# Performance work log

Hardware: AMD Instinct MI355X
Metric: run time of the kernel (lower is better)

## Reference

```python
import jax, jax.numpy as jnp
import numpy as np
from jax import lax

B = 65536

def _conv3(x, w, b):
    # x: [B,Cin,H,W], w: [Cout,Cin,3,3] (OIHW), SAME padding, stride 1
    y = lax.conv_general_dilated(x, w, (1, 1), 'SAME',
                                 dimension_numbers=('NCHW', 'OIHW', 'NCHW'))
    return y + b[None, :, None, None]

def _gru_cell(x, h, wu, bu, wr, br, wo, bo):
    s = jnp.concatenate([x, h], axis=1)
    update = jax.nn.sigmoid(_conv3(s, wu, bu))
    reset = jax.nn.sigmoid(_conv3(s, wr, br))
    out = jnp.tanh(_conv3(jnp.concatenate([x, h * reset], axis=1), wo, bo))
    return h * (1.0 - update) + out * update

def _mk_cell_params(key, cin, ch):
    ks = jax.random.split(key, 6)
    fan = (cin + ch) * 9
    sc = 1.0 / np.sqrt(fan)
    p = {}
    for i, g in enumerate(['u', 'r', 'o']):
        p['w' + g] = jax.random.normal(ks[2 * i], (ch, cin + ch, 3, 3), jnp.float32) * sc
        p['b' + g] = jax.random.normal(ks[2 * i + 1], (ch,), jnp.float32) * sc
    return p

def setup_inputs() -> dict:
    key = jax.random.key(0)
    k_in, k1, k2, k3, kd1, kd2 = jax.random.split(key, 6)
    inputs = jax.random.normal(k_in, (B, 1, 3, 3), jnp.float32)
    p1 = _mk_cell_params(k1, 1, 32)
    p2 = _mk_cell_params(k2, 32, 64)
    p3 = _mk_cell_params(k3, 64, 16)
    wd = jax.random.normal(kd1, (9, 16 * 3 * 3), jnp.float32) * (1.0 / 12.0)
    bd = jax.random.normal(kd2, (9,), jnp.float32) * (1.0 / 12.0)
    out = {'inputs': inputs, 'wd': wd, 'bd': bd}
    for i, p in enumerate([p1, p2, p3], start=1):
        for k, v in p.items():
            out[f'{k[0]}{i}{k[1]}'] = v  # e.g. w1u, b1u
    return out

def reference(inputs, wd, bd,
              w1u, b1u, w1r, b1r, w1o, b1o,
              w2u, b2u, w2r, b2r, w2o, b2o,
              w3u, b3u, w3r, b3r, w3o, b3o):
    b = inputs.shape[0]
    h1 = jnp.zeros((b, 32, 3, 3), inputs.dtype)
    h2 = jnp.zeros((b, 64, 3, 3), inputs.dtype)
    h3 = jnp.zeros((b, 16, 3, 3), inputs.dtype)
    x1 = _gru_cell(inputs, h1, w1u, b1u, w1r, b1r, w1o, b1o)
    x2 = _gru_cell(x1, h2, w2u, b2u, w2r, b2r, w2o, b2o)
    x3 = _gru_cell(x2, h3, w3u, b3u, w3r, b3r, w3o, b3o)
    out = x3.reshape(b, -1) @ wd.T + bd
    return (out, x1, x2, x3)
```

## Files before the change

kernel.cpp:

```cpp
#include <hip/hip_runtime.h>

#define BATCH 65536

typedef __attribute__((ext_vector_type(8))) short bf16x8;
typedef __attribute__((ext_vector_type(4))) float f32x4;

__device__ __forceinline__ unsigned short f2bf(float f) {
  unsigned int u = __float_as_uint(f);
  u += 0x7fffu + ((u >> 16) & 1u);
  return (unsigned short)(u >> 16);
}
__device__ __forceinline__ unsigned pack_trunc(float lo, float hi) {
  return __builtin_amdgcn_perm(__float_as_uint(hi), __float_as_uint(lo), 0x07060302u);
}

__device__ __forceinline__ float gru_act(float u, float o) {
  u = fmaxf(u, -60.0f);
  o = fmaxf(o, -30.0f);
  float a  = __expf(-u);
  float a2 = __expf(-2.0f * o);
  return (1.0f - a2) * __builtin_amdgcn_rcpf((1.0f + a) * (1.0f + a2));
}

__device__ __forceinline__ float conv_tap(const float* __restrict__ w, int co, int ci,
                                          int p, int q, int CINTOT) {
  int pi = p / 3, pj = p % 3, qi = q / 3, qj = q % 3;
  int di = qi - pi + 1, dj = qj - pj + 1;
  if ((unsigned)di < 3u && (unsigned)dj < 3u)
    return w[((co * CINTOT + ci) * 3 + di) * 3 + dj];
  return 0.0f;
}

__global__ void build_bt(const float* __restrict__ wu, const float* __restrict__ wo,
                         unsigned short* __restrict__ BT, int COUT, int CINX, int CINTOT) {
  int NG = COUT * 9, K = CINX * 9;
  int total = 2 * NG * K;
  int e = blockIdx.x * 256 + threadIdx.x;
  if (e >= total) return;
  int g = e / (NG * K);
  int rem = e - g * (NG * K);
  int n = rem / K, k = rem - n * K;
  BT[e] = f2bf(conv_tap(g ? wo : wu, n / 9, k / 9, n % 9, k % 9, CINTOT));
}

__global__ void build_a1(const float* __restrict__ wu, const float* __restrict__ wo,
                         float* __restrict__ A1) {
  int e = blockIdx.x * 256 + threadIdx.x;
  if (e >= 5184) return;
  int g = e / 2592;
  int rem = e - g * 2592;
  int q = rem / 288, c = rem - q * 288;
  A1[e] = conv_tap(g ? wo : wu, c / 9, 0, c % 9, q, 33);
}

#define OFF_X1L 0
#define OFF_X3L 0
#define OFF_WL 20480
#define OFF_BLB 25664
#define OFF_BL 40960
#define OFF_XL 65536
#define OFF_AL 65536
#define SMEM_BYTES 69632

__global__ __launch_bounds__(256, 2) void megafused(
    const float* __restrict__ xin, const float* __restrict__ A1,
    const float* __restrict__ b1u, const float* __restrict__ b1o,
    const unsigned short* __restrict__ BT2,
    const float* __restrict__ b2u, const float* __restrict__ b2o,
    const unsigned short* __restrict__ BT3,
    const float* __restrict__ b3u, const float* __restrict__ b3o,
    const float* __restrict__ wd, const float* __restrict__ bd,
    float* __restrict__ x1, float* __restrict__ x2,
    float* __restrict__ x3, float* __restrict__ out) {
  __shared__ __align__(16) char smem[SMEM_BYTES];
  char* x1l = smem + OFF_X1L;
  char* Bl = smem + OFF_BL;
  char* Al = smem + OFF_AL;
  unsigned short* x3l = (unsigned short*)(smem + OFF_X3L);
  float* xl = (float*)(smem + OFF_XL);
  float* wl = (float*)(smem + OFF_WL);
  float* blb = (float*)(smem + OFF_BLB);

  const int tid = threadIdx.x;
  const int lane = tid & 63;
  const int wid = tid >> 6;
  const int lrow = lane & 15;
  const int jc = lane >> 4;
  const int r0 = blockIdx.x * 64;
  const int srow = tid >> 2, spart = tid & 3;

  unsigned toffB2[6];
  char* wB2[6];
#pragma unroll
  for (int ci = 0; ci < 6; ++ci) {
    int row = ci * 64 + srow;
    int bg = (row < 192) ? row : (384 + row);
    toffB2[ci] = (unsigned)bg * 288u + spart * 8;
    wB2[ci] = Bl + row * 64 + ((spart ^ ((row >> 1) & 3)) << 4);
  }

  for (int c = tid; c < 576; c += 256) xl[(c / 9) * 12 + (c % 9)] = xin[(size_t)r0 * 9 + c];
  __syncthreads();

  bf16x8 pf[6];
#pragma unroll
  for (int ci = 0; ci < 6; ++ci) pf[ci] = *(const bf16x8*)(BT2 + toffB2[ci]);

  {
    float au0[9], ao0[9], au1[9], ao1[9];
    const int c1 = tid, c2 = tid + 256;
    const bool has2 = (c2 < 288);
#pragma unroll
    for (int q = 0; q < 9; ++q) {
      au0[q] = A1[q * 288 + c1];
      ao0[q] = A1[2592 + q * 288 + c1];
      au1[q] = has2 ? A1[q * 288 + c2] : 0.0f;
      ao1[q] = has2 ? A1[2592 + q * 288 + c2] : 0.0f;
    }
    float bu0 = b1u[c1 / 9], bo0 = b1o[c1 / 9];
    float bu1 = has2 ? b1u[c2 / 9] : 0.0f;
    float bo1 = has2 ? b1o[c2 / 9] : 0.0f;
    for (int r = 0; r < 64; ++r) {
      const float4 xv0 = *(const float4*)&xl[r * 12];
      const float4 xv1 = *(const float4*)&xl[r * 12 + 4];
      const float x8 = xl[r * 12 + 8];
      float u0 = bu0, o0 = bo0, u1 = bu1, o1 = bo1;
      u0 = fmaf(au0[0], xv0.x, u0); o0 = fmaf(ao0[0], xv0.x, o0);
      u0 = fmaf(au0[1], xv0.y, u0); o0 = fmaf(ao0[1], xv0.y, o0);
      u0 = fmaf(au0[2], xv0.z, u0); o0 = fmaf(ao0[2], xv0.z, o0);
      u0 = fmaf(au0[3], xv0.w, u0); o0 = fmaf(ao0[3], xv0.w, o0);
      u0 = fmaf(au0[4], xv1.x, u0); o0 = fmaf(ao0[4], xv1.x, o0);
      u0 = fmaf(au0[5], xv1.y, u0); o0 = fmaf(ao0[5], xv1.y, o0);
      u0 = fmaf(au0[6], xv1.z, u0); o0 = fmaf(ao0[6], xv1.z, o0);
      u0 = fmaf(au0[7], xv1.w, u0); o0 = fmaf(ao0[7], xv1.w, o0);
      u0 = fmaf(au0[8], x8, u0);    o0 = fmaf(ao0[8], x8, o0);
      float v0 = gru_act(u0, o0);
      x1[(size_t)(r0 + r) * 288 + c1] = v0;
      *(unsigned short*)(x1l + r * 640 + (((c1 >> 3) ^ (r & 7)) << 4) + (c1 & 7) * 2) =
          (unsigned short)(__float_as_uint(v0) >> 16);
      if (has2) {
        u1 = fmaf(au1[0], xv0.x, u1); o1 = fmaf(ao1[0], xv0.x, o1);
        u1 = fmaf(au1[1], xv0.y, u1); o1 = fmaf(ao1[1], xv0.y, o1);
        u1 = fmaf(au1[2], xv0.z, u1); o1 = fmaf(ao1[2], xv0.z, o1);
        u1 = fmaf(au1[3], xv0.w, u1); o1 = fmaf(ao1[3], xv0.w, o1);
        u1 = fmaf(au1[4], xv1.x, u1); o1 = fmaf(ao1[4], xv1.x, o1);
        u1 = fmaf(au1[5], xv1.y, u1); o1 = fmaf(ao1[5], xv1.y, o1);
        u1 = fmaf(au1[6], xv1.z, u1); o1 = fmaf(ao1[6], xv1.z, o1);
        u1 = fmaf(au1[7], xv1.w, u1); o1 = fmaf(ao1[7], xv1.w, o1);
        u1 = fmaf(au1[8], x8, u1);    o1 = fmaf(ao1[8], x8, o1);
        float v1 = gru_act(u1, o1);
        x1[(size_t)(r0 + r) * 288 + c2] = v1;
        *(unsigned short*)(x1l + r * 640 + (((c2 >> 3) ^ (r & 7)) << 4) + (c2 & 7) * 2) =
            (unsigned short)(__float_as_uint(v1) >> 16);
      }
    }
  }

  {
    const char* rB[2][3];
#pragma unroll
    for (int g = 0; g < 2; ++g)
#pragma unroll
      for (int f = 0; f < 3; ++f) {
        int rb = g * 192 + (wid * 3 + f) * 16 + lrow;
        rB[g][f] = Bl + rb * 64 + ((jc ^ ((rb >> 1) & 3)) << 4);
      }
    const char* aBase[4];
    int aXor[4];
#pragma unroll
    for (int m = 0; m < 4; ++m) {
      int row = m * 16 + lrow;
      aBase[m] = x1l + row * 640;
      aXor[m] = row & 7;
    }

    f32x4 acc[4][2][3] = {};
    for (int s = 0; s < 27; ++s) {
      const int kt = s - (s / 9) * 9;
#pragma unroll
      for (int ci = 0; ci < 6; ++ci) *(bf16x8*)wB2[ci] = pf[ci];
      __syncthreads();
      if (s < 26) {
        int ns = s + 1;
        unsigned uoff = (unsigned)(ns / 9) * 55296u + (unsigned)(ns % 9) * 32u;
#pragma unroll
        for (int ci = 0; ci < 6; ++ci)
          pf[ci] = *(const bf16x8*)(BT2 + uoff + toffB2[ci]);
      }
      bf16x8 af[4];
      const int c8 = kt * 4 + jc;
#pragma unroll
      for (int m = 0; m < 4; ++m)
        af[m] = *(const bf16x8*)(aBase[m] + ((c8 ^ aXor[m]) << 4));
      bf16x8 bfr[2][3];
#pragma unroll
      for (int g = 0; g < 2; ++g)
#pragma unroll
        for (int f = 0; f < 3; ++f) bfr[g][f] = *(const bf16x8*)rB[g][f];
#pragma unroll
      for (int m = 0; m < 4; ++m)
#pragma unroll
        for (int g = 0; g < 2; ++g)
#pragma unroll
          for (int f = 0; f < 3; ++f)
            acc[m][g][f] = __builtin_amdgcn_mfma_f32_16x16x32_bf16(
                af[m], bfr[g][f], acc[m][g][f], 0, 0, 0);
      if (kt == 8) {
        const int n0 = (s / 9) * 192;
#pragma unroll
        for (int m = 0; m < 4; ++m)
#pragma unroll
          for (int f = 0; f < 3; ++f) {
            int n = n0 + (wid * 3 + f) * 16 + lrow;
            float bU = b2u[n / 9], bO = b2o[n / 9];
            f32x4 u = acc[m][0][f], o = acc[m][1][f];
#pragma unroll
            for (int t = 0; t < 4; ++t) {
              int r = r0 + m * 16 + jc * 4 + t;
              x2[(size_t)r * 576 + n] = gru_act(u[t] + bU, o[t] + bO);
            }
            acc[m][0][f] = (f32x4){0.f, 0.f, 0.f, 0.f};
            acc[m][1][f] = (f32x4){0.f, 0.f, 0.f, 0.f};
          }
      }
      __syncthreads();
    }
  }

  {
    unsigned toffB3[5];
    char* wB3[5];
#pragma unroll
    for (int j = 0; j < 5; ++j) {
      int c = j * 256 + tid;
      if (c < 1152) {
        int row = c >> 2, part = c & 3;
        toffB3[j] = (unsigned)row * 576u + part * 8;
        wB3[j] = Bl + row * 64 + ((part ^ ((row >> 1) & 3)) << 4);
      } else {
        toffB3[j] = 0; wB3[j] = Bl;
      }
    }
    const float* pA = x2 + (size_t)(r0 + srow) * 576 + spart * 8;
    char* wAl = Al + srow * 64 + ((spart ^ ((srow >> 1) & 3)) << 4);

    float4 pa0 = *(const float4*)pA;
    float4 pa1 = *(const float4*)(pA + 4);
    bf16x8 pb[5];
#pragma unroll
    for (int j = 0; j < 5; ++j)
      if (j * 256 + tid < 1152) pb[j] = *(const bf16x8*)(BT3 + toffB3[j]);

    for (int c = tid; c < 1296; c += 256) wl[c] = wd[c];
    if (tid < 9) blb[tid] = bd[tid];

    const char* rB3[2][3];
#pragma unroll
    for (int g = 0; g < 2; ++g)
#pragma unroll
      for (int f = 0; f < 3; ++f) {
        int rb = g * 144 + (wid * 3 + f) * 16 + lrow;
        rB3[g][f] = Bl + rb * 64 + ((jc ^ ((rb >> 1) & 3)) << 4);
      }
    const char* rA3[4];
#pragma unroll
    for (int m = 0; m < 4; ++m) {
      int row = m * 16 + lrow;
      rA3[m] = Al + row * 64 + ((jc ^ ((row >> 1) & 3)) << 4);
    }

    f32x4 acc[4][2][3] = {};
    for (int kt = 0; kt < 18; ++kt) {
      uint4 h;
      h.x = pack_trunc(pa0.x, pa0.y);
      h.y = pack_trunc(pa0.z, pa0.w);
      h.z = pack_trunc(pa1.x, pa1.y);
      h.w = pack_trunc(pa1.z, pa1.w);
      *(uint4*)wAl = h;
#pragma unroll
      for (int j = 0; j < 5; ++j)
        if (j * 256 + tid < 1152) *(bf16x8*)wB3[j] = pb[j];
      __syncthreads();
      if (kt < 17) {
        const float* gp = pA + (kt + 1) * 32;
        pa0 = *(const float4*)gp;
        pa1 = *(const float4*)(gp + 4);
        unsigned uoff = (unsigned)(kt + 1) * 32u;
#pragma unroll
        for (int j = 0; j < 5; ++j)
          if (j * 256 + tid < 1152) pb[j] = *(const bf16x8*)(BT3 + uoff + toffB3[j]);
      }
      if (wid < 3) {
        bf16x8 af[4];
#pragma unroll
        for (int m = 0; m < 4; ++m) af[m] = *(const bf16x8*)rA3[m];
        bf16x8 bfr[2][3];
#pragma unroll
        for (int g = 0; g < 2; ++g)
#pragma unroll
          for (int f = 0; f < 3; ++f) bfr[g][f] = *(const bf16x8*)rB3[g][f];
#pragma unroll
        for (int m = 0; m < 4; ++m)
#pragma unroll
          for (int g = 0; g < 2; ++g)
#pragma unroll
            for (int f = 0; f < 3; ++f)
              acc[m][g][f] = __builtin_amdgcn_mfma_f32_16x16x32_bf16(
                  af[m], bfr[g][f], acc[m][g][f], 0, 0, 0);
      }
      __syncthreads();
    }
    if (wid < 3) {
#pragma unroll
      for (int m = 0; m < 4; ++m)
#pragma unroll
        for (int f = 0; f < 3; ++f) {
          int n = (wid * 3 + f) * 16 + lrow;
          float bU = b3u[n / 9], bO = b3o[n / 9];
          f32x4 u = acc[m][0][f], o = acc[m][1][f];
#pragma unroll
          for (int t = 0; t < 4; ++t) {
            int r = m * 16 + jc * 4 + t;
            float v = gru_act(u[t] + bU, o[t] + bO);
            x3[(size_t)(r0 + r) * 144 + n] = v;
            x3l[r * 146 + n] = (unsigned short)(__float_as_uint(v) >> 16);
          }
        }
    }
  }
  __syncthreads();

  if (wid < 3) {
    int drow = lane;
    int jb = wid * 3;
    float s0 = blb[jb], s1 = blb[jb + 1], s2 = blb[jb + 2];
    for (int k = 0; k < 144; k += 2) {
      unsigned pr = *(const unsigned*)&x3l[drow * 146 + k];
      float v0 = __uint_as_float(pr << 16);
      float v1 = __uint_as_float(pr & 0xffff0000u);
      const float2 w0 = *(const float2*)&wl[jb * 144 + k];
      const float2 w1 = *(const float2*)&wl[(jb + 1) * 144 + k];
      const float2 w2 = *(const float2*)&wl[(jb + 2) * 144 + k];
      s0 = fmaf(v0, w0.x, s0); s0 = fmaf(v1, w0.y, s0);
      s1 = fmaf(v0, w1.x, s1); s1 = fmaf(v1, w1.y, s1);
      s2 = fmaf(v0, w2.x, s2); s2 = fmaf(v1, w2.y, s2);
    }
    size_t ob = (size_t)(r0 + drow) * 9 + jb;
    out[ob] = s0; out[ob + 1] = s1; out[ob + 2] = s2;
  }
}

extern "C" void kernel_launch(void* const* d_in, const int* in_sizes, int n_in,
                              void* d_out, int out_size, void* d_ws, size_t ws_size,
                              hipStream_t stream) {
  const float* inputs = (const float*)d_in[0];
  const float* wd  = (const float*)d_in[1];
  const float* bd  = (const float*)d_in[2];
  const float* w1u = (const float*)d_in[3];
  const float* b1u = (const float*)d_in[4];
  const float* w1o = (const float*)d_in[7];
  const float* b1o = (const float*)d_in[8];
  const float* w2u = (const float*)d_in[9];
  const float* b2u = (const float*)d_in[10];
  const float* w2o = (const float*)d_in[13];
  const float* b2o = (const float*)d_in[14];
  const float* w3u = (const float*)d_in[15];
  const float* b3u = (const float*)d_in[16];
  const float* w3o = (const float*)d_in[19];
  const float* b3o = (const float*)d_in[20];

  float* out = (float*)d_out;
  float* x1 = out + (size_t)BATCH * 9;
  float* x2 = x1 + (size_t)BATCH * 288;
  float* x3 = x2 + (size_t)BATCH * 576;

  unsigned short* BT2 = (unsigned short*)d_ws;
  unsigned short* BT3 = BT2 + 331776;
  float* A1 = (float*)((char*)d_ws + 995328);

  build_bt<<<1296, 256, 0, stream>>>(w2u, w2o, BT2, 64, 32, 96);
  build_bt<<<648, 256, 0, stream>>>(w3u, w3o, BT3, 16, 64, 80);
  build_a1<<<21, 256, 0, stream>>>(w1u, w1o, A1);

  megafused<<<BATCH / 64, 256, 0, stream>>>(inputs, A1, b1u, b1o, BT2, b2u, b2o,
                                            BT3, b3u, b3o, wd, bd, x1, x2, x3, out);
}
```

Before: 163.7 us.

## Double block to 512 threads and split MFMA row tiles across wave pairs

Launches the fused GRU kernel with 512 threads per block and splits each block's 64 rows into two 32-row halves across wave groups. Each wave now holds half the MFMA accumulators in layers 2 and 3. The layer-1 scalar conv and the final dense layer are also redistributed so all 8 waves share the work. The goal is more waves in flight to hide latency and fewer registers per wave, at the cost of more threads contending on each block barrier and a launch bound that may force register spills.

```diff
diff --git a/kernel.cpp b/kernel.cpp
--- a/kernel.cpp
+++ b/kernel.cpp
@@ -62,7 +62,7 @@
 #define OFF_AL 65536
 #define SMEM_BYTES 69632
 
-__global__ __launch_bounds__(256, 2) void megafused(
+__global__ __launch_bounds__(512, 4) void megafused(
     const float* __restrict__ xin, const float* __restrict__ A1,
     const float* __restrict__ b1u, const float* __restrict__ b1o,
     const unsigned short* __restrict__ BT2,
@@ -85,73 +85,61 @@
   const int lane = tid & 63;
   const int wid = tid >> 6;
   const int lrow = lane & 15;
-  const int jc = lane >> 4;
+  const int jc = (lane >> 4) & 3;
+  const int mh = wid >> 2;
+  const int cg = wid & 3;
   const int r0 = blockIdx.x * 64;
   const int srow = tid >> 2, spart = tid & 3;
 
-  unsigned toffB2[6];
-  char* wB2[6];
-#pragma unroll
-  for (int ci = 0; ci < 6; ++ci) {
-    int row = ci * 64 + srow;
+  unsigned toffB2[3];
+  char* wB2[3];
+#pragma unroll
+  for (int ci = 0; ci < 3; ++ci) {
+    int row = ci * 128 + srow;
     int bg = (row < 192) ? row : (384 + row);
     toffB2[ci] = (unsigned)bg * 288u + spart * 8;
     wB2[ci] = Bl + row * 64 + ((spart ^ ((row >> 1) & 3)) << 4);
   }
 
-  for (int c = tid; c < 576; c += 256) xl[(c / 9) * 12 + (c % 9)] = xin[(size_t)r0 * 9 + c];
+  for (int c = tid; c < 576; c += 512) xl[(c / 9) * 12 + (c % 9)] = xin[(size_t)r0 * 9 + c];
   __syncthreads();
 
-  bf16x8 pf[6];
-#pragma unroll
-  for (int ci = 0; ci < 6; ++ci) pf[ci] = *(const bf16x8*)(BT2 + toffB2[ci]);
-
-  {
-    float au0[9], ao0[9], au1[9], ao1[9];
-    const int c1 = tid, c2 = tid + 256;
-    const bool has2 = (c2 < 288);
-#pragma unroll
-    for (int q = 0; q < 9; ++q) {
-      au0[q] = A1[q * 288 + c1];
-      ao0[q] = A1[2592 + q * 288 + c1];
-      au1[q] = has2 ? A1[q * 288 + c2] : 0.0f;
-      ao1[q] = has2 ? A1[2592 + q * 288 + c2] : 0.0f;
-    }
-    float bu0 = b1u[c1 / 9], bo0 = b1o[c1 / 9];
-    float bu1 = has2 ? b1u[c2 / 9] : 0.0f;
-    float bo1 = has2 ? b1o[c2 / 9] : 0.0f;
-    for (int r = 0; r < 64; ++r) {
-      const float4 xv0 = *(const float4*)&xl[r * 12];
-      const float4 xv1 = *(const float4*)&xl[r * 12 + 4];
-      const float x8 = xl[r * 12 + 8];
-      float u0 = bu0, o0 = bo0, u1 = bu1, o1 = bo1;
-      u0 = fmaf(au0[0], xv0.x, u0); o0 = fmaf(ao0[0], xv0.x, o0);
-      u0 = fmaf(au0[1], xv0.y, u0); o0 = fmaf(ao0[1], xv0.y, o0);
-      u0 = fmaf(au0[2], xv0.z, u0); o0 = fmaf(ao0[2], xv0.z, o0);
-      u0 = fmaf(au0[3], xv0.w, u0); o0 = fmaf(ao0[3], xv0.w, o0);
-      u0 = fmaf(au0[4], xv1.x, u0); o0 = fmaf(ao0[4], xv1.x, o0);
-      u0 = fmaf(au0[5], xv1.y, u0); o0 = fmaf(ao0[5], xv1.y, o0);
-      u0 = fmaf(au0[6], xv1.z, u0); o0 = fmaf(ao0[6], xv1.z, o0);
-      u0 = fmaf(au0[7], xv1.w, u0); o0 = fmaf(ao0[7], xv1.w, o0);
-      u0 = fmaf(au0[8], x8, u0);    o0 = fmaf(ao0[8], x8, o0);
-      float v0 = gru_act(u0, o0);
-      x1[(size_t)(r0 + r) * 288 + c1] = v0;
-      *(unsigned short*)(x1l + r * 640 + (((c1 >> 3) ^ (r & 7)) << 4) + (c1 & 7) * 2) =
-          (unsigned short)(__float_as_uint(v0) >> 16);
-      if (has2) {
-        u1 = fmaf(au1[0], xv0.x, u1); o1 = fmaf(ao1[0], xv0.x, o1);
-        u1 = fmaf(au1[1], xv0.y, u1); o1 = fmaf(ao1[1], xv0.y, o1);
-        u1 = fmaf(au1[2], xv0.z, u1); o1 = fmaf(ao1[2], xv0.z, o1);
-        u1 = fmaf(au1[3], xv0.w, u1); o1 = fmaf(ao1[3], xv0.w, o1);
-        u1 = fmaf(au1[4], xv1.x, u1); o1 = fmaf(ao1[4], xv1.x, o1);
-        u1 = fmaf(au1[5], xv1.y, u1); o1 = fmaf(ao1[5], xv1.y, o1);
-        u1 = fmaf(au1[6], xv1.z, u1); o1 = fmaf(ao1[6], xv1.z, o1);
-        u1 = fmaf(au1[7], xv1.w, u1); o1 = fmaf(ao1[7], xv1.w, o1);
-        u1 = fmaf(au1[8], x8, u1);    o1 = fmaf(ao1[8], x8, o1);
-        float v1 = gru_act(u1, o1);
-        x1[(size_t)(r0 + r) * 288 + c2] = v1;
-        *(unsigned short*)(x1l + r * 640 + (((c2 >> 3) ^ (r & 7)) << 4) + (c2 & 7) * 2) =
-            (unsigned short)(__float_as_uint(v1) >> 16);
+  bf16x8 pf[3];
+#pragma unroll
+  for (int ci = 0; ci < 3; ++ci) pf[ci] = *(const bf16x8*)(BT2 + toffB2[ci]);
+
+  for (int uu = 0; uu < 3; ++uu) {
+    int u = tid + (uu << 9);
+    if (u < 1152) {
+      int c = u >> 2, rq = u & 3;
+      float au[9], ao[9];
+#pragma unroll
+      for (int q = 0; q < 9; ++q) {
+        au[q] = A1[q * 288 + c];
+        ao[q] = A1[2592 + q * 288 + c];
+      }
+      float bU = b1u[c / 9], bO = b1o[c / 9];
+      const int cbase = c >> 3, cb = (c & 7) * 2;
+#pragma unroll 4
+      for (int i = 0; i < 16; ++i) {
+        int r = (rq << 4) + i;
+        const float4 xv0 = *(const float4*)&xl[r * 12];
+        const float4 xv1 = *(const float4*)&xl[r * 12 + 4];
+        const float x8 = xl[r * 12 + 8];
+        float uacc = bU, oacc = bO;
+        uacc = fmaf(au[0], xv0.x, uacc); oacc = fmaf(ao[0], xv0.x, oacc);
+        uacc = fmaf(au[1], xv0.y, uacc); oacc = fmaf(ao[1], xv0.y, oacc);
+        uacc = fmaf(au[2], xv0.z, uacc); oacc = fmaf(ao[2], xv0.z, oacc);
+        uacc = fmaf(au[3], xv0.w, uacc); oacc = fmaf(ao[3], xv0.w, oacc);
+        uacc = fmaf(au[4], xv1.x, uacc); oacc = fmaf(ao[4], xv1.x, oacc);
+        uacc = fmaf(au[5], xv1.y, uacc); oacc = fmaf(ao[5], xv1.y, oacc);
+        uacc = fmaf(au[6], xv1.z, uacc); oacc = fmaf(ao[6], xv1.z, oacc);
+        uacc = fmaf(au[7], xv1.w, uacc); oacc = fmaf(ao[7], xv1.w, oacc);
+        uacc = fmaf(au[8], x8, uacc);    oacc = fmaf(ao[8], x8, oacc);
+        float v = gru_act(uacc, oacc);
+        x1[(size_t)(r0 + r) * 288 + c] = v;
+        *(unsigned short*)(x1l + r * 640 + ((cbase ^ (r & 7)) << 4) + cb) =
+            (unsigned short)(__float_as_uint(v) >> 16);
       }
     }
   }
@@ -162,35 +150,35 @@
     for (int g = 0; g < 2; ++g)
 #pragma unroll
       for (int f = 0; f < 3; ++f) {
-        int rb = g * 192 + (wid * 3 + f) * 16 + lrow;
+        int rb = g * 192 + (cg * 3 + f) * 16 + lrow;
         rB[g][f] = Bl + rb * 64 + ((jc ^ ((rb >> 1) & 3)) << 4);
       }
-    const char* aBase[4];
-    int aXor[4];
-#pragma unroll
-    for (int m = 0; m < 4; ++m) {
-      int row = m * 16 + lrow;
+    const char* aBase[2];
+    int aXor[2];
+#pragma unroll
+    for (int m = 0; m < 2; ++m) {
+      int row = mh * 32 + m * 16 + lrow;
       aBase[m] = x1l + row * 640;
       aXor[m] = row & 7;
     }
 
-    f32x4 acc[4][2][3] = {};
+    f32x4 acc[2][2][3] = {};
     for (int s = 0; s < 27; ++s) {
       const int kt = s - (s / 9) * 9;
 #pragma unroll
-      for (int ci = 0; ci < 6; ++ci) *(bf16x8*)wB2[ci] = pf[ci];
+      for (int ci = 0; ci < 3; ++ci) *(bf16x8*)wB2[ci] = pf[ci];
       __syncthreads();
       if (s < 26) {
         int ns = s + 1;
         unsigned uoff = (unsigned)(ns / 9) * 55296u + (unsigned)(ns % 9) * 32u;
 #pragma unroll
-        for (int ci = 0; ci < 6; ++ci)
+        for (int ci = 0; ci < 3; ++ci)
           pf[ci] = *(const bf16x8*)(BT2 + uoff + toffB2[ci]);
       }
-      bf16x8 af[4];
+      bf16x8 af[2];
       const int c8 = kt * 4 + jc;
 #pragma unroll
-      for (int m = 0; m < 4; ++m)
+      for (int m = 0; m < 2; ++m)
         af[m] = *(const bf16x8*)(aBase[m] + ((c8 ^ aXor[m]) << 4));
       bf16x8 bfr[2][3];
 #pragma unroll
@@ -198,7 +186,7 @@
 #pragma unroll
         for (int f = 0; f < 3; ++f) bfr[g][f] = *(const bf16x8*)rB[g][f];
 #pragma unroll
-      for (int m = 0; m < 4; ++m)
+      for (int m = 0; m < 2; ++m)
 #pragma unroll
         for (int g = 0; g < 2; ++g)
 #pragma unroll
@@ -208,15 +196,15 @@
       if (kt == 8) {
         const int n0 = (s / 9) * 192;
 #pragma unroll
-        for (int m = 0; m < 4; ++m)
+        for (int m = 0; m < 2; ++m)
 #pragma unroll
           for (int f = 0; f < 3; ++f) {
-            int n = n0 + (wid * 3 + f) * 16 + lrow;
+            int n = n0 + (cg * 3 + f) * 16 + lrow;
             float bU = b2u[n / 9], bO = b2o[n / 9];
             f32x4 u = acc[m][0][f], o = acc[m][1][f];
 #pragma unroll
             for (int t = 0; t < 4; ++t) {
-              int r = r0 + m * 16 + jc * 4 + t;
+              int r = r0 + mh * 32 + m * 16 + jc * 4 + t;
               x2[(size_t)r * 576 + n] = gru_act(u[t] + bU, o[t] + bO);
             }
             acc[m][0][f] = (f32x4){0.f, 0.f, 0.f, 0.f};
@@ -228,30 +216,33 @@
   }
 
   {
-    unsigned toffB3[5];
-    char* wB3[5];
-#pragma unroll
-    for (int j = 0; j < 5; ++j) {
-      int c = j * 256 + tid;
-      if (c < 1152) {
-        int row = c >> 2, part = c & 3;
-        toffB3[j] = (unsigned)row * 576u + part * 8;
-        wB3[j] = Bl + row * 64 + ((part ^ ((row >> 1) & 3)) << 4);
-      } else {
-        toffB3[j] = 0; wB3[j] = Bl;
-      }
-    }
-    const float* pA = x2 + (size_t)(r0 + srow) * 576 + spart * 8;
-    char* wAl = Al + srow * 64 + ((spart ^ ((srow >> 1) & 3)) << 4);
-
-    float4 pa0 = *(const float4*)pA;
-    float4 pa1 = *(const float4*)(pA + 4);
-    bf16x8 pb[5];
-#pragma unroll
-    for (int j = 0; j < 5; ++j)
-      if (j * 256 + tid < 1152) pb[j] = *(const bf16x8*)(BT3 + toffB3[j]);
-
-    for (int c = tid; c < 1296; c += 256) wl[c] = wd[c];
+    unsigned toffB3[3];
+    char* wB3[3];
+    bool vB3[3];
+#pragma unroll
+    for (int ci = 0; ci < 3; ++ci) {
+      int row = ci * 128 + srow;
+      int g = row >= 192;
+      int nloc = row - (g ? 192 : 0);
+      vB3[ci] = (nloc < 144);
+      toffB3[ci] = (unsigned)((g ? 144 : 0) + nloc) * 576u + spart * 8;
+      wB3[ci] = Bl + row * 64 + ((spart ^ ((row >> 1) & 3)) << 4);
+    }
+    const float* pA = x2 + (size_t)(r0 + (tid >> 2)) * 576 + spart * 8;
+    char* wAl = Al + (tid >> 2) * 64 + ((spart ^ (((tid >> 2) >> 1) & 3)) << 4);
+
+    float4 pa0 = {}, pa1 = {};
+    if (tid < 256) {
+      pa0 = *(const float4*)pA;
+      pa1 = *(const float4*)(pA + 4);
+    }
+    bf16x8 pb[3];
+#pragma unroll
+    for (int ci = 0; ci < 3; ++ci)
+      pb[ci] = vB3[ci] ? *(const bf16x8*)(BT3 + toffB3[ci])
+                       : (bf16x8){0, 0, 0, 0, 0, 0, 0, 0};
+
+    for (int c = tid; c < 1296; c += 512) wl[c] = wd[c];
     if (tid < 9) blb[tid] = bd[tid];
 
     const char* rB3[2][3];
@@ -259,68 +250,69 @@
     for (int g = 0; g < 2; ++g)
 #pragma unroll
       for (int f = 0; f < 3; ++f) {
-        int rb = g * 144 + (wid * 3 + f) * 16 + lrow;
+        int rb = g * 192 + (cg * 3 + f) * 16 + lrow;
         rB3[g][f] = Bl + rb * 64 + ((jc ^ ((rb >> 1) & 3)) << 4);
       }
-    const char* rA3[4];
-#pragma unroll
-    for (int m = 0; m < 4; ++m) {
-      int row = m * 16 + lrow;
+    const char* rA3[2];
+#pragma unroll
+    for (int m = 0; m < 2; ++m) {
+      int row = mh * 32 + m * 16 + lrow;
       rA3[m] = Al + row * 64 + ((jc ^ ((row >> 1) & 3)) << 4);
     }
 
-    f32x4 acc[4][2][3] = {};
+    f32x4 acc[2][2][3] = {};
     for (int kt = 0; kt < 18; ++kt) {
-      uint4 h;
-      h.x = pack_trunc(pa0.x, pa0.y);
-      h.y = pack_trunc(pa0.z, pa0.w);
-      h.z = pack_trunc(pa1.x, pa1.y);
-      h.w = pack_trunc(pa1.z, pa1.w);
-      *(uint4*)wAl = h;
-#pragma unroll
-      for (int j = 0; j < 5; ++j)
-        if (j * 256 + tid < 1152) *(bf16x8*)wB3[j] = pb[j];
+      if (tid < 256) {
+        uint4 h;
+        h.x = pack_trunc(pa0.x, pa0.y);
+        h.y = pack_trunc(pa0.z, pa0.w);
+        h.z = pack_trunc(pa1.x, pa1.y);
+        h.w = pack_trunc(pa1.z, pa1.w);
+        *(uint4*)wAl = h;
+      }
+#pragma unroll
+      for (int ci = 0; ci < 3; ++ci) *(bf16x8*)wB3[ci] = pb[ci];
       __syncthreads();
       if (kt < 17) {
-        const float* gp = pA + (kt + 1) * 32;
-        pa0 = *(const float4*)gp;
-        pa1 = *(const float4*)(gp + 4);
+        if (tid < 256) {
+          const float* gp = pA + (kt + 1) * 32;
+          pa0 = *(const float4*)gp;
+          pa1 = *(const float4*)(gp + 4);
+        }
         unsigned uoff = (unsigned)(kt + 1) * 32u;
 #pragma unroll
-        for (int j = 0; j < 5; ++j)
-          if (j * 256 + tid < 1152) pb[j] = *(const bf16x8*)(BT3 + uoff + toffB3[j]);
-      }
-      if (wid < 3) {
-        bf16x8 af[4];
-#pragma unroll
-        for (int m = 0; m < 4; ++m) af[m] = *(const bf16x8*)rA3[m];
-        bf16x8 bfr[2][3];
+        for (int ci = 0; ci < 3; ++ci)
+          if (vB3[ci]) pb[ci] = *(const bf16x8*)(BT3 + uoff + toffB3[ci]);
+      }
+      bf16x8 af[2];
+#pragma unroll
+      for (int m = 0; m < 2; ++m) af[m] = *(const bf16x8*)rA3[m];
+      bf16x8 bfr[2][3];
+#pragma unroll
+      for (int g = 0; g < 2; ++g)
+#pragma unroll
+        for (int f = 0; f < 3; ++f) bfr[g][f] = *(const bf16x8*)rB3[g][f];
+#pragma unroll
+      for (int m = 0; m < 2; ++m)
 #pragma unroll
         for (int g = 0; g < 2; ++g)
 #pragma unroll
-          for (int f = 0; f < 3; ++f) bfr[g][f] = *(const bf16x8*)rB3[g][f];
-#pragma unroll
-        for (int m = 0; m < 4; ++m)
-#pragma unroll
-          for (int g = 0; g < 2; ++g)
-#pragma unroll
-            for (int f = 0; f < 3; ++f)
-              acc[m][g][f] = __builtin_amdgcn_mfma_f32_16x16x32_bf16(
-                  af[m], bfr[g][f], acc[m][g][f], 0, 0, 0);
-      }
+          for (int f = 0; f < 3; ++f)
+            acc[m][g][f] = __builtin_amdgcn_mfma_f32_16x16x32_bf16(
+                af[m], bfr[g][f], acc[m][g][f], 0, 0, 0);
       __syncthreads();
     }
-    if (wid < 3) {
-#pragma unroll
-      for (int m = 0; m < 4; ++m)
+    if (cg < 3) {
+#pragma unroll
+      for (int m = 0; m < 2; ++m)
 #pragma unroll
         for (int f = 0; f < 3; ++f) {
-          int n = (wid * 3 + f) * 16 + lrow;
+          int n = (cg * 3 + f) * 16 + lrow;
           float bU = b3u[n / 9], bO = b3o[n / 9];
           f32x4 u = acc[m][0][f], o = acc[m][1][f];
 #pragma unroll
           for (int t = 0; t < 4; ++t) {
-            int r = m * 16 + jc * 4 + t;
+            int r = mh * 32 + m * 16 + jc * 4 + t;
             float v = gru_act(u[t] + bU, o[t] + bO);
             x3[(size_t)(r0 + r) * 144 + n] = v;
             x3l[r * 146 + n] = (unsigned short)(__float_as_uint(v) >> 16);
@@ -330,23 +322,31 @@
   }
   __syncthreads();
 
-  if (wid < 3) {
-    int drow = lane;
-    int jb = wid * 3;
-    float s0 = blb[jb], s1 = blb[jb + 1], s2 = blb[jb + 2];
+  {
+    int row = lane;
+    int j = wid;
+    float s = blb[j];
     for (int k = 0; k < 144; k += 2) {
-      unsigned pr = *(const unsigned*)&x3l[drow * 146 + k];
+      unsigned pr = *(const unsigned*)&x3l[row * 146 + k];
       float v0 = __uint_as_float(pr << 16);
       float v1 = __uint_as_float(pr & 0xffff0000u);
-      const float2 w0 = *(const float2*)&wl[jb * 144 + k];
-      const float2 w1 = *(const float2*)&wl[(jb + 1) * 144 + k];
-      const float2 w2 = *(const float2*)&wl[(jb + 2) * 144 + k];
-      s0 = fmaf(v0, w0.x, s0); s0 = fmaf(v1, w0.y, s0);
-      s1 = fmaf(v0, w1.x, s1); s1 = fmaf(v1, w1.y, s1);
-      s2 = fmaf(v0, w2.x, s2); s2 = fmaf(v1, w2.y, s2);
-    }
-    size_t ob = (size_t)(r0 + drow) * 9 + jb;
-    out[ob] = s0; out[ob + 1] = s1; out[ob + 2] = s2;
+      const float2 w0 = *(const float2*)&wl[j * 144 + k];
+      s = fmaf(v0, w0.x, s);
+      s = fmaf(v1, w0.y, s);
+    }
+    out[(size_t)(r0 + row) * 9 + j] = s;
+    if (tid < 64) {
+      float s8 = blb[8];
+      for (int k = 0; k < 144; k += 2) {
+        unsigned pr = *(const unsigned*)&x3l[row * 146 + k];
+        float v0 = __uint_as_float(pr << 16);
+        float v1 = __uint_as_float(pr & 0xffff0000u);
+        const float2 w0 = *(const float2*)&wl[8 * 144 + k];
+        s8 = fmaf(v0, w0.x, s8);
+        s8 = fmaf(v1, w0.y, s8);
+      }
+      out[(size_t)(r0 + row) * 9 + 8] = s8;
+    }
   }
 }
 
@@ -382,6 +382,6 @@
   build_bt<<<648, 256, 0, stream>>>(w3u, w3o, BT3, 16, 64, 80);
   build_a1<<<21, 256, 0, stream>>>(w1u, w1o, A1);
 
-  megafused<<<BATCH / 64, 256, 0, stream>>>(inputs, A1, b1u, b1o, BT2, b2u, b2o,
+  megafused<<<BATCH / 64, 512, 0, stream>>>(inputs, A1, b1u, b1o, BT2, b2u, b2o,
                                             BT3, b3u, b3o, wd, bd, x1, x2, x3, out);
 }
```

Result: no change. 163.5 us (-0.1%).

## Compute first GRU layer with bf16 MFMA instead of scalar FMA loops

Applied to the files above, without the earlier changes.

Replaces the first-cell scalar FP32 FMA loop (9 taps per output, 64 rows per thread) with a bf16 MFMA GEMM. The input is padded to K=32 and the cell-1 weights are packed into a bf16 transposed matrix by a new build kernel, then processed in two 144-column chunks. The layer-3 B-tile offsets and the decoder weight staging are reused or moved earlier. This trades some FP32 accuracy in layer 1 for bf16 inputs and raises shared memory use, which could affect occupancy at two blocks per CU.

```diff
diff --git a/kernel.cpp b/kernel.cpp
--- a/kernel.cpp
+++ b/kernel.cpp
@@ -43,14 +43,15 @@
   BT[e] = f2bf(conv_tap(g ? wo : wu, n / 9, k / 9, n % 9, k % 9, CINTOT));
 }
 
-__global__ void build_a1(const float* __restrict__ wu, const float* __restrict__ wo,
-                         float* __restrict__ A1) {
+__global__ void build_bt1(const float* __restrict__ wu, const float* __restrict__ wo,
+                          unsigned short* __restrict__ BT1) {
   int e = blockIdx.x * 256 + threadIdx.x;
-  if (e >= 5184) return;
-  int g = e / 2592;
-  int rem = e - g * 2592;
-  int q = rem / 288, c = rem - q * 288;
-  A1[e] = conv_tap(g ? wo : wu, c / 9, 0, c % 9, q, 33);
+  if (e >= 18432) return;
+  int g = e / 9216;
+  int rem = e - g * 9216;
+  int n = rem / 32, k = rem - n * 32;
+  float v = (k < 9) ? conv_tap(g ? wo : wu, n / 9, 0, n % 9, k, 33) : 0.0f;
+  BT1[e] = f2bf(v);
 }
 
 #define OFF_X1L 0
@@ -58,12 +59,12 @@
 #define OFF_WL 20480
 #define OFF_BLB 25664
 #define OFF_BL 40960
-#define OFF_XL 65536
+#define OFF_XL2 65536
 #define OFF_AL 65536
-#define SMEM_BYTES 69632
+#define SMEM_BYTES 74752
 
 __global__ __launch_bounds__(256, 2) void megafused(
-    const float* __restrict__ xin, const float* __restrict__ A1,
+    const float* __restrict__ xin, const unsigned short* __restrict__ BT1,
     const float* __restrict__ b1u, const float* __restrict__ b1o,
     const unsigned short* __restrict__ BT2,
     const float* __restrict__ b2u, const float* __restrict__ b2o,
@@ -77,7 +78,7 @@
   char* Bl = smem + OFF_BL;
   char* Al = smem + OFF_AL;
   unsigned short* x3l = (unsigned short*)(smem + OFF_X3L);
-  float* xl = (float*)(smem + OFF_XL);
+  float* xl2 = (float*)(smem + OFF_XL2);
   float* wl = (float*)(smem + OFF_WL);
   float* blb = (float*)(smem + OFF_BLB);
 
@@ -90,80 +91,119 @@
   const int srow = tid >> 2, spart = tid & 3;
 
   unsigned toffB2[6];
-  char* wB2[6];
+  int wOffB2[6];
 #pragma unroll
   for (int ci = 0; ci < 6; ++ci) {
     int row = ci * 64 + srow;
     int bg = (row < 192) ? row : (384 + row);
     toffB2[ci] = (unsigned)bg * 288u + spart * 8;
-    wB2[ci] = Bl + row * 64 + ((spart ^ ((row >> 1) & 3)) << 4);
-  }
-
-  for (int c = tid; c < 576; c += 256) xl[(c / 9) * 12 + (c % 9)] = xin[(size_t)r0 * 9 + c];
+    wOffB2[ci] = row * 64 + ((spart ^ ((row >> 1) & 3)) << 4);
+  }
+  unsigned toffB1[5];
+  int wOffG[5];
+#pragma unroll
+  for (int j = 0; j < 5; ++j) {
+    int c = j * 256 + tid;
+    if (c < 1152) {
+      int row = c >> 2, p = c & 3;
+      int g = row >= 144, nloc = row - (g ? 144 : 0);
+      toffB1[j] = (unsigned)(g * 288 + nloc) * 32u + p * 8;
+      wOffG[j] = row * 64 + ((p ^ ((row >> 1) & 3)) << 4);
+    } else {
+      toffB1[j] = 0; wOffG[j] = 0;
+    }
+  }
+
+  for (int c = tid; c < 2304; c += 256) {
+    int row = c / 36, col = c - row * 36;
+    xl2[c] = (col < 9) ? xin[(size_t)(r0 + row) * 9 + col] : 0.0f;
+  }
+  bf16x8 pb[5];
+#pragma unroll
+  for (int j = 0; j < 5; ++j)
+    if (j * 256 + tid < 1152) pb[j] = *(const bf16x8*)(BT1 + toffB1[j]);
   __syncthreads();
 
+  bf16x8 afx[4];
+#pragma unroll
+  for (int m = 0; m < 4; ++m) {
+    const float* xr = xl2 + (m * 16 + lrow) * 36 + jc * 8;
+    float4 a0 = *(const float4*)xr;
+    float4 a1 = *(const float4*)(xr + 4);
+    union { uint4 u; bf16x8 v; } cv;
+    cv.u.x = pack_trunc(a0.x, a0.y);
+    cv.u.y = pack_trunc(a0.z, a0.w);
+    cv.u.z = pack_trunc(a1.x, a1.y);
+    cv.u.w = pack_trunc(a1.z, a1.w);
+    afx[m] = cv.v;
+  }
+  int rBoffG[2][3];
+#pragma unroll
+  for (int g = 0; g < 2; ++g)
+#pragma unroll
+    for (int f = 0; f < 3; ++f) {
+      int rb = g * 144 + (wid * 3 + f) * 16 + lrow;
+      rBoffG[g][f] = rb * 64 + ((jc ^ ((rb >> 1) & 3)) << 4);
+    }
+
   bf16x8 pf[6];
 #pragma unroll
-  for (int ci = 0; ci < 6; ++ci) pf[ci] = *(const bf16x8*)(BT2 + toffB2[ci]);
+  for (int ch = 0; ch < 2; ++ch) {
+#pragma unroll
+    for (int j = 0; j < 5; ++j)
+      if (j * 256 + tid < 1152) *(bf16x8*)(Bl + wOffG[j]) = pb[j];
+    if (ch == 0) {
+#pragma unroll
+      for (int j = 0; j < 5; ++j)
+        if (j * 256 + tid < 1152) pb[j] = *(const bf16x8*)(BT1 + 4608u + toffB1[j]);
+    } else {
+#pragma unroll
+      for (int q = 0; q < 6; ++q) pf[q] = *(const bf16x8*)(BT2 + toffB2[q]);
+    }
+    __syncthreads();
+    if (wid < 3) {
+      f32x4 acc[4][2][3] = {};
+      bf16x8 bfr[2][3];
+#pragma unroll
+      for (int g = 0; g < 2; ++g)
+#pragma unroll
+        for (int f = 0; f < 3; ++f) bfr[g][f] = *(const bf16x8*)(Bl + rBoffG[g][f]);
+#pragma unroll
+      for (int m = 0; m < 4; ++m)
+#pragma unroll
+        for (int g = 0; g < 2; ++g)
+#pragma unroll
+          for (int f = 0; f < 3; ++f)
+            acc[m][g][f] = __builtin_amdgcn_mfma_f32_16x16x32_bf16(
+                afx[m], bfr[g][f], acc[m][g][f], 0, 0, 0);
+#pragma unroll
+      for (int m = 0; m < 4; ++m)
+#pragma unroll
+        for (int f = 0; f < 3; ++f) {
+          int n = ch * 144 + (wid * 3 + f) * 16 + lrow;
+          float bU = b1u[n / 9], bO = b1o[n / 9];
+          f32x4 uv = acc[m][0][f], ov = acc[m][1][f];
+#pragma unroll
+          for (int t = 0; t < 4; ++t) {
+            int r = m * 16 + jc * 4 + t;
+            float v = gru_act(uv[t] + bU, ov[t] + bO);
+            x1[(size_t)(r0 + r) * 288 + n] = v;
+            *(unsigned short*)(x1l + r * 640 + (((n >> 3) ^ (r & 7)) << 4) + (n & 7) * 2) =
+                (unsigned short)(__float_as_uint(v) >> 16);
+          }
+        }
+    }
+    __syncthreads();
+  }
 
   {
-    float au0[9], ao0[9], au1[9], ao1[9];
-    const int c1 = tid, c2 = tid + 256;
-    const bool has2 = (c2 < 288);
-#pragma unroll
-    for (int q = 0; q < 9; ++q) {
-      au0[q] = A1[q * 288 + c1];
-      ao0[q] = A1[2592 + q * 288 + c1];
-      au1[q] = has2 ? A1[q * 288 + c2] : 0.0f;
-      ao1[q] = has2 ? A1[2592 + q * 288 + c2] : 0.0f;
-    }
-    float bu0 = b1u[c1 / 9], bo0 = b1o[c1 / 9];
-    float bu1 = has2 ? b1u[c2 / 9] : 0.0f;
-    float bo1 = has2 ? b1o[c2 / 9] : 0.0f;
-    for (int r = 0; r < 64; ++r) {
-      const float4 xv0 = *(const float4*)&xl[r * 12];
-      const float4 xv1 = *(const float4*)&xl[r * 12 + 4];
-      const float x8 = xl[r * 12 + 8];
-      float u0 = bu0, o0 = bo0, u1 = bu1, o1 = bo1;
-      u0 = fmaf(au0[0], xv0.x, u0); o0 = fmaf(ao0[0], xv0.x, o0);
-      u0 = fmaf(au0[1], xv0.y, u0); o0 = fmaf(ao0[1], xv0.y, o0);
-      u0 = fmaf(au0[2], xv0.z, u0); o0 = fmaf(ao0[2], xv0.z, o0);
-      u0 = fmaf(au0[3], xv0.w, u0); o0 = fmaf(ao0[3], xv0.w, o0);
-      u0 = fmaf(au0[4], xv1.x, u0); o0 = fmaf(ao0[4], xv1.x, o0);
-      u0 = fmaf(au0[5], xv1.y, u0); o0 = fmaf(ao0[5], xv1.y, o0);
-      u0 = fmaf(au0[6], xv1.z, u0); o0 = fmaf(ao0[6], xv1.z, o0);
-      u0 = fmaf(au0[7], xv1.w, u0); o0 = fmaf(ao0[7], xv1.w, o0);
-      u0 = fmaf(au0[8], x8, u0);    o0 = fmaf(ao0[8], x8, o0);
-      float v0 = gru_act(u0, o0);
-      x1[(size_t)(r0 + r) * 288 + c1] = v0;
-      *(unsigned short*)(x1l + r * 640 + (((c1 >> 3) ^ (r & 7)) << 4) + (c1 & 7) * 2) =
-          (unsigned short)(__float_as_uint(v0) >> 16);
-      if (has2) {
-        u1 = fmaf(au1[0], xv0.x, u1); o1 = fmaf(ao1[0], xv0.x, o1);
-        u1 = fmaf(au1[1], xv0.y, u1); o1 = fmaf(ao1[1], xv0.y, o1);
-        u1 = fmaf(au1[2], xv0.z, u1); o1 = fmaf(ao1[2], xv0.z, o1);
-        u1 = fmaf(au1[3], xv0.w, u1); o1 = fmaf(ao1[3], xv0.w, o1);
-        u1 = fmaf(au1[4], xv1.x, u1); o1 = fmaf(ao1[4], xv1.x, o1);
-        u1 = fmaf(au1[5], xv1.y, u1); o1 = fmaf(ao1[5], xv1.y, o1);
-        u1 = fmaf(au1[6], xv1.z, u1); o1 = fmaf(ao1[6], xv1.z, o1);
-        u1 = fmaf(au1[7], xv1.w, u1); o1 = fmaf(ao1[7], xv1.w, o1);
-        u1 = fmaf(au1[8], x8, u1);    o1 = fmaf(ao1[8], x8, o1);
-        float v1 = gru_act(u1, o1);
-        x1[(size_t)(r0 + r) * 288 + c2] = v1;
-        *(unsigned short*)(x1l + r * 640 + (((c2 >> 3) ^ (r & 7)) << 4) + (c2 & 7) * 2) =
-            (unsigned short)(__float_as_uint(v1) >> 16);
-      }
-    }
-  }
-
-  {
-    const char* rB[2][3];
+    int rBoff[2][3];
 #pragma unroll
     for (int g = 0; g < 2; ++g)
 #pragma unroll
       for (int f = 0; f < 3; ++f) {
         int rb = g * 192 + (wid * 3 + f) * 16 + lrow;
-        rB[g][f] = Bl + rb * 64 + ((jc ^ ((rb >> 1) & 3)) << 4);
+        rBoff[g][f] = rb * 64 + ((jc ^ ((rb >> 1) & 3)) << 4);
       }
     const char* aBase[4];
     int aXor[4];
@@ -178,7 +218,7 @@
     for (int s = 0; s < 27; ++s) {
       const int kt = s - (s / 9) * 9;
 #pragma unroll
-      for (int ci = 0; ci < 6; ++ci) *(bf16x8*)wB2[ci] = pf[ci];
+      for (int ci = 0; ci < 6; ++ci) *(bf16x8*)(Bl + wOffB2[ci]) = pf[ci];
       __syncthreads();
       if (s < 26) {
         int ns = s + 1;
@@ -196,7 +236,7 @@
 #pragma unroll
       for (int g = 0; g < 2; ++g)
 #pragma unroll
-        for (int f = 0; f < 3; ++f) bfr[g][f] = *(const bf16x8*)rB[g][f];
+        for (int f = 0; f < 3; ++f) bfr[g][f] = *(const bf16x8*)(Bl + rBoff[g][f]);
 #pragma unroll
       for (int m = 0; m < 4; ++m)
 #pragma unroll
@@ -213,11 +253,11 @@
           for (int f = 0; f < 3; ++f) {
             int n = n0 + (wid * 3 + f) * 16 + lrow;
             float bU = b2u[n / 9], bO = b2o[n / 9];
-            f32x4 u = acc[m][0][f], o = acc[m][1][f];
+            f32x4 uv = acc[m][0][f], ov = acc[m][1][f];
 #pragma unroll
             for (int t = 0; t < 4; ++t) {
               int r = r0 + m * 16 + jc * 4 + t;
-              x2[(size_t)r * 576 + n] = gru_act(u[t] + bU, o[t] + bO);
+              x2[(size_t)r * 576 + n] = gru_act(uv[t] + bU, ov[t] + bO);
             }
             acc[m][0][f] = (f32x4){0.f, 0.f, 0.f, 0.f};
             acc[m][1][f] = (f32x4){0.f, 0.f, 0.f, 0.f};
@@ -226,42 +266,28 @@
       __syncthreads();
     }
   }
+  __syncthreads();
+
+  for (int c = tid; c < 1296; c += 256) wl[c] = wd[c];
+  if (tid < 9) blb[tid] = bd[tid];
 
   {
     unsigned toffB3[5];
-    char* wB3[5];
 #pragma unroll
     for (int j = 0; j < 5; ++j) {
       int c = j * 256 + tid;
-      if (c < 1152) {
-        int row = c >> 2, part = c & 3;
-        toffB3[j] = (unsigned)row * 576u + part * 8;
-        wB3[j] = Bl + row * 64 + ((part ^ ((row >> 1) & 3)) << 4);
-      } else {
-        toffB3[j] = 0; wB3[j] = Bl;
-      }
+      toffB3[j] = (c < 1152) ? ((unsigned)(c >> 2) * 576u + (c & 3) * 8) : 0u;
     }
     const float* pA = x2 + (size_t)(r0 + srow) * 576 + spart * 8;
     char* wAl = Al + srow * 64 + ((spart ^ ((srow >> 1) & 3)) << 4);
 
     float4 pa0 = *(const float4*)pA;
     float4 pa1 = *(const float4*)(pA + 4);
-    bf16x8 pb[5];
+    bf16x8 pb3[5];
 #pragma unroll
     for (int j = 0; j < 5; ++j)
-      if (j * 256 + tid < 1152) pb[j] = *(const bf16x8*)(BT3 + toffB3[j]);
-
-    for (int c = tid; c < 1296; c += 256) wl[c] = wd[c];
-    if (tid < 9) blb[tid] = bd[tid];
-
-    const char* rB3[2][3];
-#pragma unroll
-    for (int g = 0; g < 2; ++g)
-#pragma unroll
-      for (int f = 0; f < 3; ++f) {
-        int rb = g * 144 + (wid * 3 + f) * 16 + lrow;
-        rB3[g][f] = Bl + rb * 64 + ((jc ^ ((rb >> 1) & 3)) << 4);
-      }
+      if (j * 256 + tid < 1152) pb3[j] = *(const bf16x8*)(BT3 + toffB3[j]);
+
     const char* rA3[4];
 #pragma unroll
     for (int m = 0; m < 4; ++m) {
@@ -279,7 +305,7 @@
       *(uint4*)wAl = h;
 #pragma unroll
       for (int j = 0; j < 5; ++j)
-        if (j * 256 + tid < 1152) *(bf16x8*)wB3[j] = pb[j];
+        if (j * 256 + tid < 1152) *(bf16x8*)(Bl + wOffG[j]) = pb3[j];
       __syncthreads();
       if (kt < 17) {
         const float* gp = pA + (kt + 1) * 32;
@@ -288,7 +314,7 @@
         unsigned uoff = (unsigned)(kt + 1) * 32u;
 #pragma unroll
         for (int j = 0; j < 5; ++j)
-          if (j * 256 + tid < 1152) pb[j] = *(const bf16x8*)(BT3 + uoff + toffB3[j]);
+          if (j * 256 + tid < 1152) pb3[j] = *(const bf16x8*)(BT3 + uoff + toffB3[j]);
       }
       if (wid < 3) {
         bf16x8 af[4];
@@ -298,7 +324,7 @@
 #pragma unroll
         for (int g = 0; g < 2; ++g)
 #pragma unroll
-          for (int f = 0; f < 3; ++f) bfr[g][f] = *(const bf16x8*)rB3[g][f];
+          for (int f = 0; f < 3; ++f) bfr[g][f] = *(const bf16x8*)(Bl + rBoffG[g][f]);
 #pragma unroll
         for (int m = 0; m < 4; ++m)
 #pragma unroll
@@ -317,11 +343,11 @@
         for (int f = 0; f < 3; ++f) {
           int n = (wid * 3 + f) * 16 + lrow;
           float bU = b3u[n / 9], bO = b3o[n / 9];
-          f32x4 u = acc[m][0][f], o = acc[m][1][f];
+          f32x4 uv = acc[m][0][f], ov = acc[m][1][f];
 #pragma unroll
           for (int t = 0; t < 4; ++t) {
             int r = m * 16 + jc * 4 + t;
-            float v = gru_act(u[t] + bU, o[t] + bO);
+            float v = gru_act(uv[t] + bU, ov[t] + bO);
             x3[(size_t)(r0 + r) * 144 + n] = v;
             x3l[r * 146 + n] = (unsigned short)(__float_as_uint(v) >> 16);
           }
@@ -376,12 +402,12 @@
 
   unsigned short* BT2 = (unsigned short*)d_ws;
   unsigned short* BT3 = BT2 + 331776;
-  float* A1 = (float*)((char*)d_ws + 995328);
+  unsigned short* BT1 = BT3 + 165888;
 
   build_bt<<<1296, 256, 0, stream>>>(w2u, w2o, BT2, 64, 32, 96);
   build_bt<<<648, 256, 0, stream>>>(w3u, w3o, BT3, 16, 64, 80);
-  build_a1<<<21, 256, 0, stream>>>(w1u, w1o, A1);
-
-  megafused<<<BATCH / 64, 256, 0, stream>>>(inputs, A1, b1u, b1o, BT2, b2u, b2o,
+  build_bt1<<<72, 256, 0, stream>>>(w1u, w1o, BT1);
+
+  megafused<<<BATCH / 64, 256, 0, stream>>>(inputs, BT1, b1u, b1o, BT2, b2u, b2o,
                                             BT3, b3u, b3o, wd, bd, x1, x2, x3, out);
 }
```

Measured after the change: 154.8 us. 5.5% less time.
